# Kernel optimization log

Hardware: AMD Instinct MI355X
Metric: run time of the kernel (lower is better)

## Reference

```python
import jax, jax.numpy as jnp
import numpy as np

BATCH, E = 4096, 8
DIMS = [512, 1024, 1024, 512]


def setup_inputs() -> dict:
    key = jax.random.key(0)
    ks = jax.random.split(key, 8)
    inp = {
        'weight_blend': jax.random.uniform(ks[0], (BATCH, E), dtype=jnp.float32),
        'x': jax.random.normal(ks[1], (BATCH, DIMS[0]), dtype=jnp.float32),
    }
    for i in range(3):
        inp[f'W{i}'] = jax.random.normal(ks[2 + i], (E, DIMS[i + 1], DIMS[i]), dtype=jnp.float32)
        inp[f'B{i}'] = jnp.zeros((E, DIMS[i + 1]), dtype=jnp.float32)
    return inp


def _blended_layer(weight_blend, x, W, B):
    # Fused form of: weight = sum_e blend[b,e]*W[e]; y = bmm(weight, x) + sum_e blend[b,e]*B[e]
    # Computed as sum_e blend_e * (W_e @ x) without materializing (batch,out,in).
    y = jnp.einsum('eoi,bi->beo', W, x)          # per-expert GEMM, (B,E,out)
    y = jnp.einsum('be,beo->bo', weight_blend, y)  # blend combine
    return y + weight_blend @ B                   # blended bias (B,out)


def reference(weight_blend, x, W0, B0, W1, B1, W2, B2):
    # Dropout with keep_prob=0.0 is identity in eval mode; activations: elu, elu, linear.
    h = jax.nn.elu(_blended_layer(weight_blend, x, W0, B0))
    h = jax.nn.elu(_blended_layer(weight_blend, h, W1, B1))
    out = _blended_layer(weight_blend, h, W2, B2)
    return out
```

## Files before the change

kernel.cpp:

```cpp
#include <hip/hip_runtime.h>
#include <cstdint>
#include <cstddef>

typedef __bf16 bf16x8 __attribute__((ext_vector_type(8)));
typedef float f32x4 __attribute__((ext_vector_type(4)));
typedef unsigned short u16;
typedef unsigned short u16x8 __attribute__((ext_vector_type(8)));

#define BATCH 4096
#define NE 8

__device__ __forceinline__ u16 f2bf(float f) {
  union { float f; uint32_t u; } v; v.f = f;
  uint32_t u = v.u;
  u += 0x7fffu + ((u >> 16) & 1u);
  return (u16)(u >> 16);
}

__device__ __forceinline__ float bf2f(u16 u) {
  union { uint32_t u; float f; } v; v.u = ((uint32_t)u) << 16;
  return v.f;
}

__device__ __forceinline__ void cast8(const float* src, u16* dst) {
  const float4* p = (const float4*)src;
  float4 a = p[0], b = p[1];
  u16x8 o;
  o[0] = f2bf(a.x); o[1] = f2bf(a.y); o[2] = f2bf(a.z); o[3] = f2bf(a.w);
  o[4] = f2bf(b.x); o[5] = f2bf(b.y); o[6] = f2bf(b.z); o[7] = f2bf(b.w);
  *(u16x8*)dst = o;
}

__device__ __forceinline__ void conv_w_chunk(const float* __restrict__ W,
                                             u16* __restrict__ Bt,
                                             int N, int K0, int chunk) {
  int per_row = K0 >> 3;
  int rid = chunk / per_row;
  int i0 = (chunk - rid * per_row) << 3;
  int e = rid / N;
  int o = rid - e * N;
  cast8(W + (size_t)rid * K0 + i0,
        Bt + (size_t)o * ((size_t)NE * K0) + (size_t)e * K0 + i0);
}

__global__ void prep_kernel(const float* __restrict__ blend,
                            const float* __restrict__ x,
                            const float* __restrict__ W0,
                            const float* __restrict__ W1,
                            const float* __restrict__ W2,
                            u16* __restrict__ hh0, u16* __restrict__ Bt0,
                            u16* __restrict__ Bt1, u16* __restrict__ Bt2) {
  int t = blockIdx.x * blockDim.x + threadIdx.x;
  const int C0 = BATCH * 512 / 8;
  const int C1 = C0 + NE * 1024 * 512 / 8;
  const int C2 = C1 + NE * 1024 * 1024 / 8;
  if (t < C0) {
    int b = t >> 6, i0 = (t & 63) << 3;
    const float4* xp = (const float4*)(x + (size_t)b * 512 + i0);
    float4 a = xp[0], c = xp[1];
    float xv[8] = {a.x, a.y, a.z, a.w, c.x, c.y, c.z, c.w};
    const float4* blp = (const float4*)(blend + (size_t)b * NE);
    float4 u0 = blp[0], u1 = blp[1];
    float bl[8] = {u0.x, u0.y, u0.z, u0.w, u1.x, u1.y, u1.z, u1.w};
    u16* dst = hh0 + (size_t)b * 4096 + i0;
    #pragma unroll
    for (int e = 0; e < NE; ++e) {
      u16x8 o;
      #pragma unroll
      for (int j = 0; j < 8; ++j) o[j] = f2bf(bl[e] * xv[j]);
      *(u16x8*)(dst + (size_t)e * 512) = o;
    }
  } else if (t < C1) {
    conv_w_chunk(W0, Bt0, 1024, 512, t - C0);
  } else if (t < C2) {
    conv_w_chunk(W1, Bt1, 1024, 1024, t - C1);
  } else {
    conv_w_chunk(W2, Bt2, 512, 1024, t - C2);
  }
}

template<int SLICES, bool ELU_ACT, int OM>
__global__ void combineS_kernel(const u16* __restrict__ P,
                                const float* __restrict__ blend,
                                const float* __restrict__ Bias,
                                void* __restrict__ outp, int N) {
  int t = blockIdx.x * blockDim.x + threadIdx.x;
  int per_row = N >> 3;
  int b = t / per_row;
  int i0 = (t - b * per_row) << 3;
  const size_t slice = (size_t)BATCH * N;
  float v[8] = {0, 0, 0, 0, 0, 0, 0, 0};
  #pragma unroll
  for (int s = 0; s < SLICES; ++s) {
    u16x8 pv = *(const u16x8*)(P + (size_t)s * slice + (size_t)b * N + i0);
    #pragma unroll
    for (int j = 0; j < 8; ++j) v[j] += bf2f(pv[j]);
  }
  const float4* blp = (const float4*)(blend + b * NE);
  float4 u0 = blp[0], u1 = blp[1];
  float bl[8] = {u0.x, u0.y, u0.z, u0.w, u1.x, u1.y, u1.z, u1.w};
  #pragma unroll
  for (int e = 0; e < NE; ++e) {
    const float4* bp = (const float4*)(Bias + (size_t)e * N + i0);
    float4 ba = bp[0], bb = bp[1];
    float bv[8] = {ba.x, ba.y, ba.z, ba.w, bb.x, bb.y, bb.z, bb.w};
    #pragma unroll
    for (int j = 0; j < 8; ++j) v[j] += bl[e] * bv[j];
  }
  if (ELU_ACT) {
    #pragma unroll
    for (int j = 0; j < 8; ++j) v[j] = v[j] > 0.f ? v[j] : expm1f(v[j]);
  }
  if (OM == 1) {
    u16* hh = (u16*)outp;
    size_t base = (size_t)b * ((size_t)NE * N) + i0;
    #pragma unroll
    for (int e = 0; e < NE; ++e) {
      u16x8 o;
      #pragma unroll
      for (int j = 0; j < 8; ++j) o[j] = f2bf(bl[e] * v[j]);
      *(u16x8*)(hh + base + (size_t)e * N) = o;
    }
  } else {
    float4* op = (float4*)((float*)outp + (size_t)b * N + i0);
    op[0] = (float4){v[0], v[1], v[2], v[3]};
    op[1] = (float4){v[4], v[5], v[6], v[7]};
  }
}

#define GL2LDS(g, l) __builtin_amdgcn_global_load_lds( \
    (__attribute__((address_space(1))) void*)(g),      \
    (__attribute__((address_space(3))) void*)(l), 16, 0, 0)

#define SBAR  asm volatile("s_barrier" ::: "memory")
#define VMW6  asm volatile("s_waitcnt vmcnt(6)" ::: "memory")

template<int NT>
__global__ __launch_bounds__(512, 2)
void gemm8p_kernel(const u16* __restrict__ A, const u16* __restrict__ B,
                   u16* __restrict__ P, int N, int KTOT, int KSL) {
  __shared__ __align__(16) char SM[131072];

  const int tid  = threadIdx.x;
  const int lane = tid & 63, w = tid >> 6;
  const int wm   = w >> 2, wn = w & 3;
  const int lrow = lane & 15, quad = lane >> 4;

  const int row0 = blockIdx.x * 256;
  const int col0 = blockIdx.y * 256;
  const size_t kb0 = (size_t)blockIdx.z * KSL;

  const int sr = tid >> 3, sc = tid & 7;
  const int tcol = sc ^ (sr & 7);
  const u16* gA = A + ((size_t)(row0 + sr) * KTOT + kb0 + (tcol << 3));
  const u16* gB = B + ((size_t)(col0 + sr) * KTOT + kb0 + (tcol << 3));

#define STA(T, q, BUF) GL2LDS(gA + (size_t)(64 * (q)) * KTOT + (size_t)(T) * 64, \
                              SM + (BUF) * 65536 + (q) * 8192 + (size_t)tid * 16)
#define STB(T, q, BUF) GL2LDS(gB + (size_t)(64 * (q)) * KTOT + (size_t)(T) * 64, \
                              SM + (BUF) * 65536 + 32768 + (q) * 8192 + (size_t)tid * 16)

  const int xr = lrow & 7;
  const uint32_t arow = (uint32_t)((wm * 128 + lrow) * 128);
  const uint32_t brow = (uint32_t)((wn * 64 + lrow) * 128);
  uint32_t ch[2];
  ch[0] = (uint32_t)((quad ^ xr) << 4);
  ch[1] = (uint32_t)(((4 + quad) ^ xr) << 4);

  f32x4 acc[8][4];
  #pragma unroll
  for (int i = 0; i < 8; ++i)
    #pragma unroll
    for (int j = 0; j < 4; ++j) acc[i][j] = (f32x4){0.f, 0.f, 0.f, 0.f};

  STA(0, 0, 0); STA(0, 1, 0); STA(0, 2, 0); STA(0, 3, 0);
  STB(0, 0, 0); STB(0, 1, 0); STB(0, 2, 0); STB(0, 3, 0);
  STB(1, 0, 1); STB(1, 1, 1); STB(1, 2, 1); STB(1, 3, 1);
  STA(1, 0, 1); STA(1, 2, 1);
  VMW6;
  SBAR;

#define PHASE(q, CUR, RDB, STAGES)                                              \
  {                                                                             \
    if (RDB) {                                                                  \
      _Pragma("unroll")                                                         \
      for (int nt = 0; nt < 4; ++nt)                                            \
        _Pragma("unroll")                                                       \
        for (int kc = 0; kc < 2; ++kc)                                          \
          bfr[nt][kc] = *(const bf16x8*)(SM + (CUR) + 32768 + brow +            \
                                         nt * 2048 + ch[kc]);                   \
    }                                                                           \
    bf16x8 af[2][2];                                                            \
    _Pragma("unroll")                                                           \
    for (int m2 = 0; m2 < 2; ++m2)                                              \
      _Pragma("unroll")                                                         \
      for (int kc = 0; kc < 2; ++kc)                                            \
        af[m2][kc] = *(const bf16x8*)(SM + (CUR) + arow +                       \
                                      ((q) * 2 + m2) * 2048 + ch[kc]);          \
    STAGES;                                                                     \
    SBAR;                                                                       \
    __builtin_amdgcn_s_setprio(1);                                              \
    _Pragma("unroll")                                                           \
    for (int kc = 0; kc < 2; ++kc)                                              \
      _Pragma("unroll")                                                         \
      for (int m2 = 0; m2 < 2; ++m2)                                            \
        _Pragma("unroll")                                                       \
        for (int nt = 0; nt < 4; ++nt)                                          \
          acc[(q) * 2 + m2][nt] = __builtin_amdgcn_mfma_f32_16x16x32_bf16(      \
              af[m2][kc], bfr[nt][kc], acc[(q) * 2 + m2][nt], 0, 0, 0);         \
    __builtin_amdgcn_s_setprio(0);                                              \
  }

  constexpr int NIT = NT / 2;
  #pragma unroll 1
  for (int j = 0; j < NIT; ++j) {
    const int u = 2 * j;
    const bool sg = (u + 2 < NT);
    bf16x8 bfr[4][2];
    PHASE(0, 0, true,  { STA(u + 1, 1, 1); STA(u + 1, 3, 1); });
    SBAR;
    PHASE(1, 0, false, { if (sg) { STB(u + 2, 0, 0); STB(u + 2, 1, 0); } });
    SBAR;
    PHASE(2, 0, false, { if (sg) { STA(u + 2, 0, 0); STA(u + 2, 2, 0); } });
    SBAR;
    PHASE(3, 0, false, { if (sg) { STB(u + 2, 2, 0); STB(u + 2, 3, 0); } });
    VMW6;
    SBAR;
    PHASE(0, 65536, true,  { if (sg) { STA(u + 2, 1, 0); STA(u + 2, 3, 0); } });
    SBAR;
    PHASE(1, 65536, false, { if (sg) { STB(u + 3, 0, 1); STB(u + 3, 1, 1); } });
    SBAR;
    PHASE(2, 65536, false, { if (sg) { STA(u + 3, 0, 1); STA(u + 3, 2, 1); } });
    SBAR;
    PHASE(3, 65536, false, { if (sg) { STB(u + 3, 2, 1); STB(u + 3, 3, 1); } });
    VMW6;
    SBAR;
  }
#undef PHASE
#undef STA
#undef STB

  u16* Ps = P + (size_t)blockIdx.z * ((size_t)BATCH * N);
  u16* ls = (u16*)SM + w * 2048;
  #pragma unroll
  for (int pass = 0; pass < 4; ++pass) {
    #pragma unroll
    for (int mh = 0; mh < 2; ++mh) {
      int mt = pass * 2 + mh;
      #pragma unroll
      for (int r = 0; r < 4; ++r) {
        int rloc = mh * 16 + quad * 4 + r;
        #pragma unroll
        for (int nt = 0; nt < 4; ++nt) {
          int col = nt * 16 + lrow;
          int c8 = (col >> 3) ^ (rloc & 7);
          ls[rloc * 64 + (c8 << 3) + (col & 7)] = f2bf(acc[mt][nt][r]);
        }
      }
    }
    #pragma unroll
    for (int p8 = 0; p8 < 4; ++p8) {
      int rloc = p8 * 8 + (lane >> 3);
      int c8 = (lane & 7) ^ (rloc & 7);
      u16x8 v = *(const u16x8*)&ls[rloc * 64 + (c8 << 3)];
      int row = row0 + wm * 128 + pass * 32 + rloc;
      int colg = col0 + wn * 64 + ((lane & 7) << 3);
      *(u16x8*)&Ps[(size_t)row * N + colg] = v;
    }
  }
}

extern "C" void kernel_launch(void* const* d_in, const int* in_sizes, int n_in,
                              void* d_out, int out_size, void* d_ws, size_t ws_size,
                              hipStream_t stream) {
  const float* blend = (const float*)d_in[0];
  const float* x  = (const float*)d_in[1];
  const float* W0 = (const float*)d_in[2];
  const float* B0 = (const float*)d_in[3];
  const float* W1 = (const float*)d_in[4];
  const float* B1 = (const float*)d_in[5];
  const float* W2 = (const float*)d_in[6];
  const float* B2 = (const float*)d_in[7];
  float* out = (float*)d_out;

  char* ws = (char*)d_ws;
  u16* hh1 = (u16*)ws;
  u16* hh0 = (u16*)(ws + 67108864);
  u16* hh2 = (u16*)(ws + 67108864);
  u16* Bt0 = (u16*)(ws + 134217728);
  u16* Bt1 = (u16*)(ws + 142606336);
  u16* Bt2 = (u16*)(ws + 159383552);
  u16* P   = (u16*)(ws + 167772160);

  prep_kernel<<<9216, 256, 0, stream>>>(blend, x, W0, W1, W2, hh0, Bt0, Bt1, Bt2);

  gemm8p_kernel<16><<<dim3(16, 4, 4), 512, 0, stream>>>(hh0, Bt0, P, 1024, 4096, 1024);
  combineS_kernel<4, true, 1><<<2048, 256, 0, stream>>>(P, blend, B0, hh1, 1024);

  gemm8p_kernel<32><<<dim3(16, 4, 4), 512, 0, stream>>>(hh1, Bt1, P, 1024, 8192, 2048);
  combineS_kernel<4, true, 1><<<2048, 256, 0, stream>>>(P, blend, B1, hh2, 1024);

  gemm8p_kernel<16><<<dim3(16, 2, 8), 512, 0, stream>>>(hh2, Bt2, P, 512, 8192, 1024);
  combineS_kernel<8, false, 0><<<1024, 256, 0, stream>>>(P, blend, B2, out, 512);
}
```

Measured before the change: 304.7 us.

## Apply blend weight in GEMM epilogue instead of expanding activations per expert

```diff
diff --git a/kernel.cpp b/kernel.cpp
--- a/kernel.cpp
+++ b/kernel.cpp
@@ -43,33 +43,18 @@
         Bt + (size_t)o * ((size_t)NE * K0) + (size_t)e * K0 + i0);
 }
 
-__global__ void prep_kernel(const float* __restrict__ blend,
-                            const float* __restrict__ x,
+__global__ void prep_kernel(const float* __restrict__ x,
                             const float* __restrict__ W0,
                             const float* __restrict__ W1,
                             const float* __restrict__ W2,
-                            u16* __restrict__ hh0, u16* __restrict__ Bt0,
+                            u16* __restrict__ h0, u16* __restrict__ Bt0,
                             u16* __restrict__ Bt1, u16* __restrict__ Bt2) {
   int t = blockIdx.x * blockDim.x + threadIdx.x;
   const int C0 = BATCH * 512 / 8;
   const int C1 = C0 + NE * 1024 * 512 / 8;
   const int C2 = C1 + NE * 1024 * 1024 / 8;
   if (t < C0) {
-    int b = t >> 6, i0 = (t & 63) << 3;
-    const float4* xp = (const float4*)(x + (size_t)b * 512 + i0);
-    float4 a = xp[0], c = xp[1];
-    float xv[8] = {a.x, a.y, a.z, a.w, c.x, c.y, c.z, c.w};
-    const float4* blp = (const float4*)(blend + (size_t)b * NE);
-    float4 u0 = blp[0], u1 = blp[1];
-    float bl[8] = {u0.x, u0.y, u0.z, u0.w, u1.x, u1.y, u1.z, u1.w};
-    u16* dst = hh0 + (size_t)b * 4096 + i0;
-    #pragma unroll
-    for (int e = 0; e < NE; ++e) {
-      u16x8 o;
-      #pragma unroll
-      for (int j = 0; j < 8; ++j) o[j] = f2bf(bl[e] * xv[j]);
-      *(u16x8*)(dst + (size_t)e * 512) = o;
-    }
+    cast8(x + (size_t)t * 8, h0 + (size_t)t * 8);
   } else if (t < C1) {
     conv_w_chunk(W0, Bt0, 1024, 512, t - C0);
   } else if (t < C2) {
@@ -79,7 +64,7 @@
   }
 }
 
-template<int SLICES, bool ELU_ACT, int OM>
+template<int SLICES, bool ELU_ACT, bool OUT_BF16>
 __global__ void combineS_kernel(const u16* __restrict__ P,
                                 const float* __restrict__ blend,
                                 const float* __restrict__ Bias,
@@ -111,16 +96,11 @@
     #pragma unroll
     for (int j = 0; j < 8; ++j) v[j] = v[j] > 0.f ? v[j] : expm1f(v[j]);
   }
-  if (OM == 1) {
-    u16* hh = (u16*)outp;
-    size_t base = (size_t)b * ((size_t)NE * N) + i0;
-    #pragma unroll
-    for (int e = 0; e < NE; ++e) {
-      u16x8 o;
-      #pragma unroll
-      for (int j = 0; j < 8; ++j) o[j] = f2bf(bl[e] * v[j]);
-      *(u16x8*)(hh + base + (size_t)e * N) = o;
-    }
+  if (OUT_BF16) {
+    u16x8 o;
+    #pragma unroll
+    for (int j = 0; j < 8; ++j) o[j] = f2bf(v[j]);
+    *(u16x8*)((u16*)outp + (size_t)b * N + i0) = o;
   } else {
     float4* op = (float4*)((float*)outp + (size_t)b * N + i0);
     op[0] = (float4){v[0], v[1], v[2], v[3]};
@@ -134,11 +114,13 @@
 
 #define SBAR  asm volatile("s_barrier" ::: "memory")
 #define VMW6  asm volatile("s_waitcnt vmcnt(6)" ::: "memory")
+#define VMW0  asm volatile("s_waitcnt vmcnt(0)" ::: "memory")
 
 template<int NT>
 __global__ __launch_bounds__(512, 2)
-void gemm8p_kernel(const u16* __restrict__ A, const u16* __restrict__ B,
-                   u16* __restrict__ P, int N, int KTOT, int KSL) {
+void gemm8p_kernel(const u16* __restrict__ A, const u16* __restrict__ Bt,
+                   const float* __restrict__ blend,
+                   u16* __restrict__ P, int N, int sA, int sB) {
   __shared__ __align__(16) char SM[131072];
 
   const int tid  = threadIdx.x;
@@ -146,18 +128,26 @@
   const int wm   = w >> 2, wn = w & 3;
   const int lrow = lane & 15, quad = lane >> 4;
 
-  const int row0 = blockIdx.x * 256;
-  const int col0 = blockIdx.y * 256;
-  const size_t kb0 = (size_t)blockIdx.z * KSL;
+  const int nx = gridDim.x, ny = gridDim.y;
+  const int nwg = nx * ny * gridDim.z;
+  const int bid = blockIdx.x + nx * (blockIdx.y + ny * blockIdx.z);
+  const int swz = (bid & 7) * (nwg >> 3) + (bid >> 3);
+  const int bx = swz % nx;
+  const int byz = swz / nx;
+  const int by = byz % ny;
+  const int bz = byz / ny;
+
+  const int row0 = bx * 256;
+  const int col0 = by * 256;
 
   const int sr = tid >> 3, sc = tid & 7;
   const int tcol = sc ^ (sr & 7);
-  const u16* gA = A + ((size_t)(row0 + sr) * KTOT + kb0 + (tcol << 3));
-  const u16* gB = B + ((size_t)(col0 + sr) * KTOT + kb0 + (tcol << 3));
-
-#define STA(T, q, BUF) GL2LDS(gA + (size_t)(64 * (q)) * KTOT + (size_t)(T) * 64, \
+  const u16* gA = A + ((size_t)(row0 + sr) * sA + (tcol << 3));
+  const u16* gB = Bt + ((size_t)(col0 + sr) * sB + (size_t)bz * (NT * 64) + (tcol << 3));
+
+#define STA(T, q, BUF) GL2LDS(gA + (size_t)(64 * (q)) * sA + (size_t)(T) * 64, \
                               SM + (BUF) * 65536 + (q) * 8192 + (size_t)tid * 16)
-#define STB(T, q, BUF) GL2LDS(gB + (size_t)(64 * (q)) * KTOT + (size_t)(T) * 64, \
+#define STB(T, q, BUF) GL2LDS(gB + (size_t)(64 * (q)) * sB + (size_t)(T) * 64, \
                               SM + (BUF) * 65536 + 32768 + (q) * 8192 + (size_t)tid * 16)
 
   const int xr = lrow & 7;
@@ -224,7 +214,7 @@
     PHASE(2, 0, false, { if (sg) { STA(u + 2, 0, 0); STA(u + 2, 2, 0); } });
     SBAR;
     PHASE(3, 0, false, { if (sg) { STB(u + 2, 2, 0); STB(u + 2, 3, 0); } });
-    VMW6;
+    if (sg) { VMW6; } else { VMW0; }
     SBAR;
     PHASE(0, 65536, true,  { if (sg) { STA(u + 2, 1, 0); STA(u + 2, 3, 0); } });
     SBAR;
@@ -240,7 +230,20 @@
 #undef STA
 #undef STB
 
-  u16* Ps = P + (size_t)blockIdx.z * ((size_t)BATCH * N);
+  {
+    const int rbase = row0 + wm * 128 + quad * 4;
+    #pragma unroll
+    for (int mt = 0; mt < 8; ++mt) {
+      #pragma unroll
+      for (int r = 0; r < 4; ++r) {
+        const float bl = blend[(size_t)(rbase + (mt >> 1) * 32 + (mt & 1) * 16 + r) * NE + bz];
+        #pragma unroll
+        for (int nt = 0; nt < 4; ++nt) acc[mt][nt][r] *= bl;
+      }
+    }
+  }
+
+  u16* Ps = P + (size_t)bz * ((size_t)BATCH * N);
   u16* ls = (u16*)SM + w * 2048;
   #pragma unroll
   for (int pass = 0; pass < 4; ++pass) {
@@ -284,22 +287,21 @@
   float* out = (float*)d_out;
 
   char* ws = (char*)d_ws;
-  u16* hh1 = (u16*)ws;
-  u16* hh0 = (u16*)(ws + 67108864);
-  u16* hh2 = (u16*)(ws + 67108864);
-  u16* Bt0 = (u16*)(ws + 134217728);
-  u16* Bt1 = (u16*)(ws + 142606336);
-  u16* Bt2 = (u16*)(ws + 159383552);
-  u16* P   = (u16*)(ws + 167772160);
-
-  prep_kernel<<<9216, 256, 0, stream>>>(blend, x, W0, W1, W2, hh0, Bt0, Bt1, Bt2);
-
-  gemm8p_kernel<16><<<dim3(16, 4, 4), 512, 0, stream>>>(hh0, Bt0, P, 1024, 4096, 1024);
-  combineS_kernel<4, true, 1><<<2048, 256, 0, stream>>>(P, blend, B0, hh1, 1024);
-
-  gemm8p_kernel<32><<<dim3(16, 4, 4), 512, 0, stream>>>(hh1, Bt1, P, 1024, 8192, 2048);
-  combineS_kernel<4, true, 1><<<2048, 256, 0, stream>>>(P, blend, B1, hh2, 1024);
-
-  gemm8p_kernel<16><<<dim3(16, 2, 8), 512, 0, stream>>>(hh2, Bt2, P, 512, 8192, 1024);
-  combineS_kernel<8, false, 0><<<1024, 256, 0, stream>>>(P, blend, B2, out, 512);
-}
+  u16* hA  = (u16*)ws;
+  u16* h1  = (u16*)(ws + 8388608);
+  u16* Bt0 = (u16*)(ws + 16777216);
+  u16* Bt1 = (u16*)(ws + 25165824);
+  u16* Bt2 = (u16*)(ws + 41943040);
+  u16* P   = (u16*)(ws + 50331648);
+
+  prep_kernel<<<9216, 256, 0, stream>>>(x, W0, W1, W2, hA, Bt0, Bt1, Bt2);
+
+  gemm8p_kernel<8><<<dim3(16, 4, 8), 512, 0, stream>>>(hA, Bt0, blend, P, 1024, 512, 4096);
+  combineS_kernel<8, true, true><<<2048, 256, 0, stream>>>(P, blend, B0, h1, 1024);
+
+  gemm8p_kernel<16><<<dim3(16, 4, 8), 512, 0, stream>>>(h1, Bt1, blend, P, 1024, 1024, 8192);
+  combineS_kernel<8, true, true><<<2048, 256, 0, stream>>>(P, blend, B1, hA, 1024);
+
+  gemm8p_kernel<16><<<dim3(16, 2, 8), 512, 0, stream>>>(hA, Bt2, blend, P, 512, 1024, 8192);
+  combineS_kernel<8, false, false><<<1024, 256, 0, stream>>>(P, blend, B2, out, 512);
+}
```

Result: no change. 309.2 us (+1.5%).
